# Kernel tuning notes

Measured on AMD Instinct MI355X. Metric: run time of the kernel, lower is better.

The kernel has to match this reference:

```python
import jax, jax.numpy as jnp
import numpy as np

N, D, E, H, O, K = 4096, 1024, 8, 2048, 1024, 2
LOSS_COEF = 0.01


def setup_inputs() -> dict:
    key = jax.random.key(0)
    ks = jax.random.split(key, 8)
    x = jax.random.normal(ks[0], (N, D), jnp.float32)
    return {
        "x": x,
        "x_offsets": jnp.array([0, N // 2, N], jnp.int32),  # unused by forward math
        "max_seq_len": 2048,
        "group_norm": False,
        "num_groups": 8,
        "linear_dim": D // 8,
        "norm_weight": jax.random.uniform(ks[1], (D,), jnp.float32, 0.5, 1.5),
        "norm_bias": jax.random.normal(ks[2], (D,), jnp.float32) * 0.1,
        "norm_eps": 1e-5,
        "w_gate": jax.random.normal(ks[3], (D, E), jnp.float32) * (1.0 / np.sqrt(D)),
        "experts_hidden_w": jax.random.normal(ks[4], (E, H, D), jnp.float32) * 0.02,
        "experts_hidden_bias": jnp.zeros((E, H), jnp.float32),
        "experts_w": jax.random.normal(ks[5], (E, O, H), jnp.float32) * 0.02,
        "experts_bias": jnp.zeros((E, O), jnp.float32),
        "output_weight": jax.random.normal(ks[6], (D, O), jnp.float32) * 0.02,
    }


def _cv_squared(v, eps=1e-6):
    v = v.astype(jnp.float32)
    m = v.mean()
    return jnp.var(v, ddof=1) / (m * m + eps)  # torch .var() is unbiased


def reference(x, x_offsets, max_seq_len, group_norm, num_groups, linear_dim,
              norm_weight, norm_bias, norm_eps,
              w_gate, experts_hidden_w, experts_hidden_bias,
              experts_w, experts_bias, output_weight):
    # ---- input normalization (layer_norm branch; group_norm=False) ----
    if group_norm:
        xg = x.reshape(-1, num_groups, linear_dim)
        mu = xg.mean(axis=2, keepdims=True)
        var = ((xg - mu) ** 2).mean(axis=2, keepdims=True)
        xg = (xg - mu) * jax.lax.rsqrt(var + norm_eps)
        xg = xg * norm_weight[None, :, None] + norm_bias[None, :, None]
        x_norm = xg.reshape(-1, x.shape[-1])
    else:
        mu = x.mean(axis=-1, keepdims=True)
        var = ((x - mu) ** 2).mean(axis=-1, keepdims=True)  # biased, like F.layer_norm
        x_norm = (x - mu) * jax.lax.rsqrt(var + norm_eps) * norm_weight + norm_bias

    # ---- gating: clean logits (enable_noisy_gating=False), L2-normalize rows ----
    logits = x_norm @ w_gate                                  # [N, E]
    logits = logits / jnp.maximum(
        jnp.linalg.norm(logits, axis=1, keepdims=True), 1e-12)
    probs = jax.nn.softmax(logits, axis=1)                    # softmax over all experts
    _, top_idx = jax.lax.top_k(logits, K)                     # [N, K]
    gates_k = jnp.take_along_axis(probs, top_idx, axis=1)     # top-k of softmax(logits)
    rows = jnp.arange(logits.shape[0])[:, None]
    gates = jnp.zeros_like(logits).at[rows, top_idx].set(gates_k)  # [N, E] sparse gates

    # ---- load-balancing loss (train=True, non-noisy path) ----
    importance = gates.sum(axis=0)
    load = (gates > 0).sum(axis=0).astype(jnp.float32)
    loss = (_cv_squared(importance) + _cv_squared(load)) * LOSS_COEF

    # ---- expert MLPs; gates are exactly zero off top-k so masked-dense == dispatch ----
    h = jax.nn.silu(jnp.einsum('nd,ehd->enh', x_norm, experts_hidden_w)
                    + experts_hidden_bias[:, None, :])        # [E, N, H]
    eo = jnp.einsum('enh,eoh->eno', h, experts_w) + experts_bias[:, None, :]  # [E, N, O]
    y_moe = jnp.einsum('ne,eno->no', gates.astype(jnp.float32),
                       eo.astype(jnp.float32))                # fp32 combine, like index_add

    # ---- residual projection: addmm(y_moe, x, output_weight) ----
    y = y_moe + x @ output_weight
    gate_fraction = load / load.sum()
    return (y, loss, gate_fraction)
```

## Files before the change

### kernel.cpp

```cpp
#include <hip/hip_runtime.h>
#include <hip/hip_bf16.h>
#include <stdint.h>

#define N_TOK 4096
#define DIM   1024
#define NE    8
#define NH    2048
#define NO    1024

typedef __attribute__((ext_vector_type(8))) short bf16x8;
typedef __attribute__((ext_vector_type(4))) float f32x4;

__device__ inline unsigned short f2bf(float f) {
    unsigned u = __float_as_uint(f);
    u += 0x7fffu + ((u >> 16) & 1u);
    return (unsigned short)(u >> 16);
}

__device__ inline void async_copy16(const void* g, void* l) {
    __builtin_amdgcn_global_load_lds(
        (const __attribute__((address_space(1))) void*)g,
        (__attribute__((address_space(3))) void*)l, 16, 0, 0);
}

__global__ __launch_bounds__(256) void ln_gate_kernel(
    const float* __restrict__ x, const float* __restrict__ nw,
    const float* __restrict__ nb, const float* __restrict__ eps_p,
    const float* __restrict__ wg,
    unsigned short* __restrict__ xn_bf, unsigned short* __restrict__ x_bf,
    int* __restrict__ tok_e, float* __restrict__ tok_g)
{
    int n = blockIdx.x;
    int t = threadIdx.x;
    int lane = t & 63, wv = t >> 6;

    const float4 xv = ((const float4*)(x + (size_t)n * DIM))[t];
    float s  = xv.x + xv.y + xv.z + xv.w;
    float s2 = xv.x*xv.x + xv.y*xv.y + xv.z*xv.z + xv.w*xv.w;
    #pragma unroll
    for (int o = 32; o > 0; o >>= 1) {
        s  += __shfl_down(s, o);
        s2 += __shfl_down(s2, o);
    }
    __shared__ float rs[4], rs2[4];
    __shared__ float gred[4][NE];
    if (lane == 0) { rs[wv] = s; rs2[wv] = s2; }
    __syncthreads();
    float S  = rs[0] + rs[1] + rs[2] + rs[3];
    float S2 = rs2[0] + rs2[1] + rs2[2] + rs2[3];
    const float inv = 1.0f / (float)DIM;
    float mu = S * inv;
    float var = fmaxf(S2 * inv - mu * mu, 0.0f);
    float rstd = rsqrtf(var + eps_p[0]);

    float4 w4 = ((const float4*)nw)[t];
    float4 b4 = ((const float4*)nb)[t];
    float xn0 = (xv.x - mu) * rstd * w4.x + b4.x;
    float xn1 = (xv.y - mu) * rstd * w4.y + b4.y;
    float xn2 = (xv.z - mu) * rstd * w4.z + b4.z;
    float xn3 = (xv.w - mu) * rstd * w4.w + b4.w;

    ushort4 pn; pn.x = f2bf(xn0); pn.y = f2bf(xn1); pn.z = f2bf(xn2); pn.w = f2bf(xn3);
    ((ushort4*)(xn_bf + (size_t)n * DIM))[t] = pn;
    ushort4 px; px.x = f2bf(xv.x); px.y = f2bf(xv.y); px.z = f2bf(xv.z); px.w = f2bf(xv.w);
    ((ushort4*)(x_bf + (size_t)n * DIM))[t] = px;

    float acc[NE];
    #pragma unroll
    for (int e = 0; e < NE; ++e) acc[e] = 0.0f;
    float xns[4] = {xn0, xn1, xn2, xn3};
    const float4* wgp = (const float4*)(wg + (size_t)(4 * t) * NE);
    #pragma unroll
    for (int j = 0; j < 4; ++j) {
        float4 w0 = wgp[2 * j], w1 = wgp[2 * j + 1];
        float xj = xns[j];
        acc[0] += xj * w0.x; acc[1] += xj * w0.y; acc[2] += xj * w0.z; acc[3] += xj * w0.w;
        acc[4] += xj * w1.x; acc[5] += xj * w1.y; acc[6] += xj * w1.z; acc[7] += xj * w1.w;
    }
    #pragma unroll
    for (int o = 32; o > 0; o >>= 1) {
        #pragma unroll
        for (int e = 0; e < NE; ++e) acc[e] += __shfl_down(acc[e], o);
    }
    if (lane == 0) {
        #pragma unroll
        for (int e = 0; e < NE; ++e) gred[wv][e] = acc[e];
    }
    __syncthreads();
    if (t == 0) {
        float lg[NE];
        float nrm2 = 0.0f;
        #pragma unroll
        for (int e = 0; e < NE; ++e) {
            lg[e] = gred[0][e] + gred[1][e] + gred[2][e] + gred[3][e];
            nrm2 += lg[e] * lg[e];
        }
        float den = fmaxf(sqrtf(nrm2), 1e-12f);
        float linv = 1.0f / den;
        #pragma unroll
        for (int e = 0; e < NE; ++e) lg[e] *= linv;
        float mx = lg[0];
        #pragma unroll
        for (int e = 1; e < NE; ++e) mx = fmaxf(mx, lg[e]);
        float p[NE], ps = 0.0f;
        #pragma unroll
        for (int e = 0; e < NE; ++e) { p[e] = expf(lg[e] - mx); ps += p[e]; }
        float pinv = 1.0f / ps;
        #pragma unroll
        for (int e = 0; e < NE; ++e) p[e] *= pinv;
        int i0 = 0; float b0 = lg[0];
        #pragma unroll
        for (int e = 1; e < NE; ++e) if (lg[e] > b0) { b0 = lg[e]; i0 = e; }
        int i1 = -1; float b1 = -3.0e38f;
        #pragma unroll
        for (int e = 0; e < NE; ++e) if (e != i0 && lg[e] > b1) { b1 = lg[e]; i1 = e; }
        tok_e[2 * n] = i0; tok_e[2 * n + 1] = i1;
        tok_g[2 * n] = p[i0]; tok_g[2 * n + 1] = p[i1];
    }
}

__global__ void cvt_bf16_kernel(const float* __restrict__ src,
                                unsigned short* __restrict__ dst, int n4) {
    int i = blockIdx.x * blockDim.x + threadIdx.x;
    if (i < n4) {
        float4 v = ((const float4*)src)[i];
        ushort4 o; o.x = f2bf(v.x); o.y = f2bf(v.y); o.z = f2bf(v.z); o.w = f2bf(v.w);
        ((ushort4*)dst)[i] = o;
    }
}

__global__ void transpose_cvt_kernel(const float* __restrict__ w,
                                     unsigned short* __restrict__ wt) {
    __shared__ float tile[32][33];
    int tx = threadIdx.x, ty = threadIdx.y;
    int o0 = blockIdx.x * 32, d0 = blockIdx.y * 32;
    tile[ty][tx] = w[(size_t)(d0 + ty) * NO + o0 + tx];
    __syncthreads();
    wt[(size_t)(o0 + ty) * DIM + d0 + tx] = f2bf(tile[tx][ty]);
}

__device__ inline float cv_sq(const float* v) {
    float m = 0.0f;
    for (int e = 0; e < NE; ++e) m += v[e];
    m *= (1.0f / NE);
    float s = 0.0f;
    for (int e = 0; e < NE; ++e) { float d = v[e] - m; s += d * d; }
    s *= (1.0f / (NE - 1));
    return s / (m * m + 1e-6f);
}

__global__ __launch_bounds__(1024) void count_finalize_kernel(
    const int* __restrict__ tok_e, const float* __restrict__ tok_g,
    int* __restrict__ counts, int* __restrict__ offsets,
    int* __restrict__ cursor_pad, float* __restrict__ out_tail)
{
    int t = threadIdx.x;
    int lane = t & 63, wv = t >> 6;
    int lc[NE]; float li[NE];
    #pragma unroll
    for (int e = 0; e < NE; ++e) { lc[e] = 0; li[e] = 0.0f; }
    const int4* ep = (const int4*)(tok_e) + 2 * t;
    const float4* gp = (const float4*)(tok_g) + 2 * t;
    #pragma unroll
    for (int q = 0; q < 2; ++q) {
        int4 e4 = ep[q]; float4 g4 = gp[q];
        lc[e4.x]++; li[e4.x] += g4.x;
        lc[e4.y]++; li[e4.y] += g4.y;
        lc[e4.z]++; li[e4.z] += g4.z;
        lc[e4.w]++; li[e4.w] += g4.w;
    }
    #pragma unroll
    for (int o = 32; o > 0; o >>= 1) {
        #pragma unroll
        for (int e = 0; e < NE; ++e) {
            lc[e] += __shfl_down(lc[e], o);
            li[e] += __shfl_down(li[e], o);
        }
    }
    __shared__ int   sc[16][NE];
    __shared__ float sf[16][NE];
    if (lane == 0) {
        #pragma unroll
        for (int e = 0; e < NE; ++e) { sc[wv][e] = lc[e]; sf[wv][e] = li[e]; }
    }
    __syncthreads();
    if (t == 0) {
        float lif[NE], lcf[NE];
        int off = 0;
        for (int e = 0; e < NE; ++e) {
            int c = 0; float im = 0.0f;
            for (int w = 0; w < 16; ++w) { c += sc[w][e]; im += sf[w][e]; }
            counts[e] = c;
            offsets[e] = off;
            cursor_pad[e * 32] = off;
            off += c;
            lcf[e] = (float)c; lif[e] = im;
        }
        float tot = (float)off;
        out_tail[0] = 0.01f * (cv_sq(lif) + cv_sq(lcf));
        for (int e = 0; e < NE; ++e) out_tail[1 + e] = lcf[e] / tot;
    }
}

__global__ __launch_bounds__(256) void scatter_kernel(
    const int* __restrict__ tok_e, int* __restrict__ cursor_pad,
    int* __restrict__ rowsbuf, int* __restrict__ pair_slot)
{
    __shared__ int lhist[NE];
    __shared__ int lbase[NE];
    int t = threadIdx.x;
    int tok0 = blockIdx.x * 512 + 2 * t;
    if (t < NE) lhist[t] = 0;
    __syncthreads();
    int4 e4 = *(const int4*)(tok_e + 2 * tok0);
    int r0 = atomicAdd(&lhist[e4.x], 1);
    int r1 = atomicAdd(&lhist[e4.y], 1);
    int r2 = atomicAdd(&lhist[e4.z], 1);
    int r3 = atomicAdd(&lhist[e4.w], 1);
    __syncthreads();
    if (t < NE) lbase[t] = atomicAdd(&cursor_pad[t * 32], lhist[t]);
    __syncthreads();
    int s0 = lbase[e4.x] + r0;
    int s1 = lbase[e4.y] + r1;
    int s2 = lbase[e4.z] + r2;
    int s3 = lbase[e4.w] + r3;
    rowsbuf[s0] = tok0;     rowsbuf[s1] = tok0;
    rowsbuf[s2] = tok0 + 1; rowsbuf[s3] = tok0 + 1;
    *(int4*)(pair_slot + 2 * tok0) = (int4){s0, s1, s2, s3};
}

#define BK 64

__global__ __launch_bounds__(256) void gemm1_kernel(
    const unsigned short* __restrict__ xn,
    const unsigned short* __restrict__ wh,
    const float* __restrict__ hb,
    const int* __restrict__ rowsbuf,
    const int* __restrict__ counts, const int* __restrict__ offsets,
    unsigned short* __restrict__ hbuf)
{
    int e = blockIdx.z;
    int count = counts[e];
    int tm = blockIdx.y, tn = blockIdx.x;
    if (tm * 128 >= count) return;
    int off = offsets[e];

    __shared__ alignas(16) short As[128 * BK];
    __shared__ alignas(16) short Bs[128 * BK];

    int t = threadIdx.x;
    int c = t & 7, rl = t >> 3;
    int csw = (c ^ (rl & 7)) * 8;
    const unsigned short* aptr[4];
    const unsigned short* bptr[4];
    #pragma unroll
    for (int p = 0; p < 4; ++p) {
        int mrow = tm * 128 + p * 32 + rl;
        int mc = mrow < count ? mrow : count - 1;
        int token = rowsbuf[off + mc];
        aptr[p] = xn + (size_t)token * DIM;
        bptr[p] = wh + ((size_t)e * NH + tn * 128 + p * 32 + rl) * DIM;
    }

    int lane = t & 63, wvi = t >> 6;
    int wm = (wvi & 1) * 64, wn = (wvi >> 1) * 64;
    int l15 = lane & 15, q = lane >> 4, sw = l15 & 7;

    f32x4 acc[4][4];
    #pragma unroll
    for (int i = 0; i < 4; ++i)
        #pragma unroll
        for (int j = 0; j < 4; ++j) acc[i][j] = (f32x4){0.f, 0.f, 0.f, 0.f};

    for (int kt = 0; kt < DIM / BK; ++kt) {
        int kb = kt * BK + csw;
        #pragma unroll
        for (int p = 0; p < 4; ++p)
            async_copy16(aptr[p] + kb, (char*)As + p * 4096 + t * 16);
        #pragma unroll
        for (int p = 0; p < 4; ++p)
            async_copy16(bptr[p] + kb, (char*)Bs + p * 4096 + t * 16);
        __syncthreads();
        #pragma unroll
        for (int ks = 0; ks < 2; ++ks) {
            int ph = ((ks * 4 + q) ^ sw) * 8;
            bf16x8 af[4], bfr[4];
            #pragma unroll
            for (int i = 0; i < 4; ++i)
                af[i] = *(const bf16x8*)&As[(wm + i * 16 + l15) * BK + ph];
            #pragma unroll
            for (int j = 0; j < 4; ++j)
                bfr[j] = *(const bf16x8*)&Bs[(wn + j * 16 + l15) * BK + ph];
            #pragma unroll
            for (int i = 0; i < 4; ++i)
                #pragma unroll
                for (int j = 0; j < 4; ++j)
                    acc[i][j] = __builtin_amdgcn_mfma_f32_16x16x32_bf16(af[i], bfr[j], acc[i][j], 0, 0, 0);
        }
        __syncthreads();
    }

    int q4 = (lane >> 4) * 4;
    #pragma unroll
    for (int i = 0; i < 4; ++i) {
        #pragma unroll
        for (int r = 0; r < 4; ++r) {
            int m = tm * 128 + wm + i * 16 + q4 + r;
            if (m < count) {
                size_t rowbase = (size_t)(off + m) * NH;
                #pragma unroll
                for (int j = 0; j < 4; ++j) {
                    int col = tn * 128 + wn + j * 16 + l15;
                    float v = acc[i][j][r] + hb[e * NH + col];
                    v = v / (1.0f + __expf(-v));
                    hbuf[rowbase + col] = f2bf(v);
                }
            }
        }
    }
}

__global__ __launch_bounds__(256) void gemm2_kernel(
    const unsigned short* __restrict__ hbuf,
    const unsigned short* __restrict__ wo,
    const float* __restrict__ ob,
    const int* __restrict__ counts, const int* __restrict__ offsets,
    float* __restrict__ eo)
{
    int e = blockIdx.z;
    int count = counts[e];
    int tm = blockIdx.y, tn = blockIdx.x;
    if (tm * 128 >= count) return;
    int off = offsets[e];

    __shared__ alignas(16) short As[128 * BK];
    __shared__ alignas(16) short Bs[64 * BK];

    int t = threadIdx.x;
    int c = t & 7, rl = t >> 3;
    int csw = (c ^ (rl & 7)) * 8;
    const unsigned short* aptr[4];
    const unsigned short* bptr[2];
    #pragma unroll
    for (int p = 0; p < 4; ++p) {
        int mrow = tm * 128 + p * 32 + rl;
        int mc = mrow < count ? mrow : count - 1;
        aptr[p] = hbuf + (size_t)(off + mc) * NH;
    }
    #pragma unroll
    for (int p = 0; p < 2; ++p)
        bptr[p] = wo + ((size_t)e * NO + tn * 64 + p * 32 + rl) * NH;

    int lane = t & 63, wvi = t >> 6;
    int wm = (wvi & 1) * 64, wn = (wvi >> 1) * 32;
    int l15 = lane & 15, q = lane >> 4, sw = l15 & 7;

    f32x4 acc[4][2];
    #pragma unroll
    for (int i = 0; i < 4; ++i)
        #pragma unroll
        for (int j = 0; j < 2; ++j) acc[i][j] = (f32x4){0.f, 0.f, 0.f, 0.f};

    for (int kt = 0; kt < NH / BK; ++kt) {
        int kb = kt * BK + csw;
        #pragma unroll
        for (int p = 0; p < 4; ++p)
            async_copy16(aptr[p] + kb, (char*)As + p * 4096 + t * 16);
        #pragma unroll
        for (int p = 0; p < 2; ++p)
            async_copy16(bptr[p] + kb, (char*)Bs + p * 4096 + t * 16);
        __syncthreads();
        #pragma unroll
        for (int ks = 0; ks < 2; ++ks) {
            int ph = ((ks * 4 + q) ^ sw) * 8;
            bf16x8 af[4], bfr[2];
            #pragma unroll
            for (int i = 0; i < 4; ++i)
                af[i] = *(const bf16x8*)&As[(wm + i * 16 + l15) * BK + ph];
            #pragma unroll
            for (int j = 0; j < 2; ++j)
                bfr[j] = *(const bf16x8*)&Bs[(wn + j * 16 + l15) * BK + ph];
            #pragma unroll
            for (int i = 0; i < 4; ++i)
                #pragma unroll
                for (int j = 0; j < 2; ++j)
                    acc[i][j] = __builtin_amdgcn_mfma_f32_16x16x32_bf16(af[i], bfr[j], acc[i][j], 0, 0, 0);
        }
        __syncthreads();
    }

    int q4 = (lane >> 4) * 4;
    #pragma unroll
    for (int i = 0; i < 4; ++i) {
        #pragma unroll
        for (int r = 0; r < 4; ++r) {
            int m = tm * 128 + wm + i * 16 + q4 + r;
            if (m < count) {
                size_t rowbase = (size_t)(off + m) * NO;
                #pragma unroll
                for (int j = 0; j < 2; ++j) {
                    int col = tn * 64 + wn + j * 16 + l15;
                    eo[rowbase + col] = acc[i][j][r] + ob[e * NO + col];
                }
            }
        }
    }
}

__global__ __launch_bounds__(256) void gemm_res_kernel(
    const unsigned short* __restrict__ xb,
    const unsigned short* __restrict__ wt,
    float* __restrict__ y)
{
    int tm = blockIdx.y, tn = blockIdx.x;
    __shared__ alignas(16) short As[64 * BK];
    __shared__ alignas(16) short Bs[128 * BK];

    int t = threadIdx.x;
    int c = t & 7, rl = t >> 3;
    int csw = (c ^ (rl & 7)) * 8;
    const unsigned short* aptr[2];
    const unsigned short* bptr[4];
    #pragma unroll
    for (int p = 0; p < 2; ++p)
        aptr[p] = xb + (size_t)(tm * 64 + p * 32 + rl) * DIM;
    #pragma unroll
    for (int p = 0; p < 4; ++p)
        bptr[p] = wt + (size_t)(tn * 128 + p * 32 + rl) * DIM;

    int lane = t & 63, wvi = t >> 6;
    int wm = (wvi & 1) * 32, wn = (wvi >> 1) * 64;
    int l15 = lane & 15, q = lane >> 4, sw = l15 & 7;

    f32x4 acc[2][4];
    #pragma unroll
    for (int i = 0; i < 2; ++i)
        #pragma unroll
        for (int j = 0; j < 4; ++j) acc[i][j] = (f32x4){0.f, 0.f, 0.f, 0.f};

    for (int kt = 0; kt < DIM / BK; ++kt) {
        int kb = kt * BK + csw;
        #pragma unroll
        for (int p = 0; p < 2; ++p)
            async_copy16(aptr[p] + kb, (char*)As + p * 4096 + t * 16);
        #pragma unroll
        for (int p = 0; p < 4; ++p)
            async_copy16(bptr[p] + kb, (char*)Bs + p * 4096 + t * 16);
        __syncthreads();
        #pragma unroll
        for (int ks = 0; ks < 2; ++ks) {
            int ph = ((ks * 4 + q) ^ sw) * 8;
            bf16x8 af[2], bfr[4];
            #pragma unroll
            for (int i = 0; i < 2; ++i)
                af[i] = *(const bf16x8*)&As[(wm + i * 16 + l15) * BK + ph];
            #pragma unroll
            for (int j = 0; j < 4; ++j)
                bfr[j] = *(const bf16x8*)&Bs[(wn + j * 16 + l15) * BK + ph];
            #pragma unroll
            for (int i = 0; i < 2; ++i)
                #pragma unroll
                for (int j = 0; j < 4; ++j)
                    acc[i][j] = __builtin_amdgcn_mfma_f32_16x16x32_bf16(af[i], bfr[j], acc[i][j], 0, 0, 0);
        }
        __syncthreads();
    }

    int q4 = (lane >> 4) * 4;
    #pragma unroll
    for (int i = 0; i < 2; ++i) {
        #pragma unroll
        for (int r = 0; r < 4; ++r) {
            int row = tm * 64 + wm + i * 16 + q4 + r;
            #pragma unroll
            for (int j = 0; j < 4; ++j) {
                int col = tn * 128 + wn + j * 16 + l15;
                y[(size_t)row * NO + col] = acc[i][j][r];
            }
        }
    }
}

__global__ __launch_bounds__(256) void combine_kernel(
    float* __restrict__ y, const float* __restrict__ eo,
    const int* __restrict__ pair_slot, const float* __restrict__ tok_g)
{
    int n = blockIdx.x, t = threadIdx.x;
    int s0 = pair_slot[2 * n], s1 = pair_slot[2 * n + 1];
    float g0 = tok_g[2 * n], g1 = tok_g[2 * n + 1];
    float4 a = ((const float4*)(eo + (size_t)s0 * NO))[t];
    float4 b = ((const float4*)(eo + (size_t)s1 * NO))[t];
    float4* yp = (float4*)(y + (size_t)n * NO) + t;
    float4 v = *yp;
    v.x += g0 * a.x + g1 * b.x;
    v.y += g0 * a.y + g1 * b.y;
    v.z += g0 * a.z + g1 * b.z;
    v.w += g0 * a.w + g1 * b.w;
    *yp = v;
}

extern "C" void kernel_launch(void* const* d_in, const int* in_sizes, int n_in,
                              void* d_out, int out_size, void* d_ws, size_t ws_size,
                              hipStream_t stream) {
    const float* x    = (const float*)d_in[0];
    const float* nw   = (const float*)d_in[6];
    const float* nb   = (const float*)d_in[7];
    const float* eps  = (const float*)d_in[8];
    const float* wg   = (const float*)d_in[9];
    const float* whw  = (const float*)d_in[10];
    const float* whb  = (const float*)d_in[11];
    const float* wow  = (const float*)d_in[12];
    const float* wob  = (const float*)d_in[13];
    const float* wout = (const float*)d_in[14];

    char* ws = (char*)d_ws;
    unsigned short* xn_bf = (unsigned short*)(ws + 0);
    unsigned short* x_bf  = (unsigned short*)(ws + 8388608);
    unsigned short* wh_bf = (unsigned short*)(ws + 16777216);
    float*          eo    = (float*)(ws + 16777216);
    unsigned short* wo_bf = (unsigned short*)(ws + 50331648);
    unsigned short* wt_bf = (unsigned short*)(ws + 83886080);
    unsigned short* hbuf  = (unsigned short*)(ws + 85983232);
    char* meta = ws + 119537664;
    int*   counts     = (int*)(meta + 0);
    int*   offsets    = (int*)(meta + 128);
    int*   cursor_pad = (int*)(meta + 256);
    int*   tok_e      = (int*)(meta + 2048);
    float* tok_g      = (float*)(meta + 2048 + 32768);
    int*   rowsbuf    = (int*)(meta + 2048 + 65536);
    int*   pair_slot  = (int*)(meta + 2048 + 98304);

    float* y = (float*)d_out;
    float* out_tail = y + (size_t)N_TOK * NO;

    ln_gate_kernel<<<N_TOK, 256, 0, stream>>>(x, nw, nb, eps, wg, xn_bf, x_bf,
                                              tok_e, tok_g);
    {
        int n4 = NE * NH * DIM / 4;
        cvt_bf16_kernel<<<n4 / 256, 256, 0, stream>>>(whw, wh_bf, n4);
        cvt_bf16_kernel<<<n4 / 256, 256, 0, stream>>>(wow, wo_bf, n4);
    }
    transpose_cvt_kernel<<<dim3(NO / 32, DIM / 32), dim3(32, 32), 0, stream>>>(wout, wt_bf);
    count_finalize_kernel<<<1, 1024, 0, stream>>>(tok_e, tok_g, counts, offsets,
                                                  cursor_pad, out_tail);
    scatter_kernel<<<N_TOK / 512, 256, 0, stream>>>(tok_e, cursor_pad, rowsbuf, pair_slot);
    gemm1_kernel<<<dim3(NH / 128, N_TOK / 128, NE), 256, 0, stream>>>(
        xn_bf, wh_bf, whb, rowsbuf, counts, offsets, hbuf);
    gemm2_kernel<<<dim3(NO / 64, N_TOK / 128, NE), 256, 0, stream>>>(
        hbuf, wo_bf, wob, counts, offsets, eo);
    gemm_res_kernel<<<dim3(NO / 128, N_TOK / 64), 256, 0, stream>>>(x_bf, wt_bf, y);
    combine_kernel<<<N_TOK, 256, 0, stream>>>(y, eo, pair_slot, tok_g);
}
```

Before: 403.0 us.

## Use 32x32x16 MFMA in GEMMs, fuse routing kernels and weight conversions

All three GEMM kernels move from 16x16x32 bf16 MFMA tiles to 32x32x16 tiles with 16-wide accumulators, which cuts the number of LDS fragment loads and MFMA issues per K step. The count/finalize and scatter kernels merge into one multi-block route kernel. Each block recomputes the global histogram and writes deterministic slots through LDS atomics, avoiding global atomics and a launch. The two weight-conversion launches are merged into one. The epilogue store pattern changes to the 32x32 accumulator layout, which may give less coalesced writes.

```diff
diff --git a/kernel.cpp b/kernel.cpp
--- a/kernel.cpp
+++ b/kernel.cpp
@@ -9,7 +9,7 @@
 #define NO    1024
 
 typedef __attribute__((ext_vector_type(8))) short bf16x8;
-typedef __attribute__((ext_vector_type(4))) float f32x4;
+typedef __attribute__((ext_vector_type(16))) float f32x16;
 
 __device__ inline unsigned short f2bf(float f) {
     unsigned u = __float_as_uint(f);
@@ -119,14 +119,16 @@
     }
 }
 
-__global__ void cvt_bf16_kernel(const float* __restrict__ src,
-                                unsigned short* __restrict__ dst, int n4) {
+__global__ void cvt2_bf16_kernel(const float* __restrict__ a, unsigned short* __restrict__ da,
+                                 const float* __restrict__ b, unsigned short* __restrict__ db,
+                                 int n4each) {
     int i = blockIdx.x * blockDim.x + threadIdx.x;
-    if (i < n4) {
-        float4 v = ((const float4*)src)[i];
-        ushort4 o; o.x = f2bf(v.x); o.y = f2bf(v.y); o.z = f2bf(v.z); o.w = f2bf(v.w);
-        ((ushort4*)dst)[i] = o;
-    }
+    const float4* s; ushort4* d; int j;
+    if (i < n4each) { s = (const float4*)a; d = (ushort4*)da; j = i; }
+    else            { s = (const float4*)b; d = (ushort4*)db; j = i - n4each; }
+    float4 v = s[j];
+    ushort4 o; o.x = f2bf(v.x); o.y = f2bf(v.y); o.z = f2bf(v.z); o.w = f2bf(v.w);
+    d[j] = o;
 }
 
 __global__ void transpose_cvt_kernel(const float* __restrict__ w,
@@ -149,84 +151,84 @@
     return s / (m * m + 1e-6f);
 }
 
-__global__ __launch_bounds__(1024) void count_finalize_kernel(
+__global__ __launch_bounds__(256) void route_kernel(
     const int* __restrict__ tok_e, const float* __restrict__ tok_g,
     int* __restrict__ counts, int* __restrict__ offsets,
-    int* __restrict__ cursor_pad, float* __restrict__ out_tail)
+    int* __restrict__ rowsbuf, int* __restrict__ pair_slot,
+    float* __restrict__ out_tail)
 {
-    int t = threadIdx.x;
+    int b = blockIdx.x, t = threadIdx.x;
     int lane = t & 63, wv = t >> 6;
+    int chunk0 = b * 1024;
+
     int lc[NE]; float li[NE];
     #pragma unroll
     for (int e = 0; e < NE; ++e) { lc[e] = 0; li[e] = 0.0f; }
-    const int4* ep = (const int4*)(tok_e) + 2 * t;
-    const float4* gp = (const float4*)(tok_g) + 2 * t;
-    #pragma unroll
-    for (int q = 0; q < 2; ++q) {
-        int4 e4 = ep[q]; float4 g4 = gp[q];
+    int base = t * 32;
+    #pragma unroll
+    for (int q = 0; q < 8; ++q) {
+        int4 e4 = *(const int4*)(tok_e + base + q * 4);
+        float4 g4 = *(const float4*)(tok_g + base + q * 4);
         lc[e4.x]++; li[e4.x] += g4.x;
         lc[e4.y]++; li[e4.y] += g4.y;
         lc[e4.z]++; li[e4.z] += g4.z;
         lc[e4.w]++; li[e4.w] += g4.w;
     }
+    int prior_flag = (base + 32 <= chunk0) ? 1 : 0;
+    int lp[NE];
+    #pragma unroll
+    for (int e = 0; e < NE; ++e) lp[e] = prior_flag ? lc[e] : 0;
+
     #pragma unroll
     for (int o = 32; o > 0; o >>= 1) {
         #pragma unroll
         for (int e = 0; e < NE; ++e) {
             lc[e] += __shfl_down(lc[e], o);
+            lp[e] += __shfl_down(lp[e], o);
             li[e] += __shfl_down(li[e], o);
         }
     }
-    __shared__ int   sc[16][NE];
-    __shared__ float sf[16][NE];
+    __shared__ int   sc[4][NE], sp[4][NE];
+    __shared__ float sf[4][NE];
+    __shared__ int   lcur[NE];
     if (lane == 0) {
         #pragma unroll
-        for (int e = 0; e < NE; ++e) { sc[wv][e] = lc[e]; sf[wv][e] = li[e]; }
+        for (int e = 0; e < NE; ++e) { sc[wv][e] = lc[e]; sp[wv][e] = lp[e]; sf[wv][e] = li[e]; }
     }
     __syncthreads();
     if (t == 0) {
-        float lif[NE], lcf[NE];
+        int cnt[NE], pri[NE]; float imp[NE];
+        for (int e = 0; e < NE; ++e) {
+            cnt[e] = sc[0][e] + sc[1][e] + sc[2][e] + sc[3][e];
+            pri[e] = sp[0][e] + sp[1][e] + sp[2][e] + sp[3][e];
+            imp[e] = sf[0][e] + sf[1][e] + sf[2][e] + sf[3][e];
+        }
         int off = 0;
         for (int e = 0; e < NE; ++e) {
-            int c = 0; float im = 0.0f;
-            for (int w = 0; w < 16; ++w) { c += sc[w][e]; im += sf[w][e]; }
-            counts[e] = c;
-            offsets[e] = off;
-            cursor_pad[e * 32] = off;
-            off += c;
-            lcf[e] = (float)c; lif[e] = im;
-        }
-        float tot = (float)off;
-        out_tail[0] = 0.01f * (cv_sq(lif) + cv_sq(lcf));
-        for (int e = 0; e < NE; ++e) out_tail[1 + e] = lcf[e] / tot;
-    }
-}
-
-__global__ __launch_bounds__(256) void scatter_kernel(
-    const int* __restrict__ tok_e, int* __restrict__ cursor_pad,
-    int* __restrict__ rowsbuf, int* __restrict__ pair_slot)
-{
-    __shared__ int lhist[NE];
-    __shared__ int lbase[NE];
-    int t = threadIdx.x;
-    int tok0 = blockIdx.x * 512 + 2 * t;
-    if (t < NE) lhist[t] = 0;
+            lcur[e] = off + pri[e];
+            if (b == 0) { counts[e] = cnt[e]; offsets[e] = off; }
+            off += cnt[e];
+        }
+        if (b == 0) {
+            float lcf[NE], lif[NE];
+            for (int e = 0; e < NE; ++e) { lcf[e] = (float)cnt[e]; lif[e] = imp[e]; }
+            float tot = (float)off;
+            out_tail[0] = 0.01f * (cv_sq(lif) + cv_sq(lcf));
+            for (int e = 0; e < NE; ++e) out_tail[1 + e] = lcf[e] / tot;
+        }
+    }
     __syncthreads();
-    int4 e4 = *(const int4*)(tok_e + 2 * tok0);
-    int r0 = atomicAdd(&lhist[e4.x], 1);
-    int r1 = atomicAdd(&lhist[e4.y], 1);
-    int r2 = atomicAdd(&lhist[e4.z], 1);
-    int r3 = atomicAdd(&lhist[e4.w], 1);
-    __syncthreads();
-    if (t < NE) lbase[t] = atomicAdd(&cursor_pad[t * 32], lhist[t]);
-    __syncthreads();
-    int s0 = lbase[e4.x] + r0;
-    int s1 = lbase[e4.y] + r1;
-    int s2 = lbase[e4.z] + r2;
-    int s3 = lbase[e4.w] + r3;
+
+    int g0 = chunk0 + 4 * t;
+    int4 e4 = *(const int4*)(tok_e + g0);
+    int s0 = atomicAdd(&lcur[e4.x], 1);
+    int s1 = atomicAdd(&lcur[e4.y], 1);
+    int s2 = atomicAdd(&lcur[e4.z], 1);
+    int s3 = atomicAdd(&lcur[e4.w], 1);
+    int tok0 = g0 >> 1;
     rowsbuf[s0] = tok0;     rowsbuf[s1] = tok0;
     rowsbuf[s2] = tok0 + 1; rowsbuf[s3] = tok0 + 1;
-    *(int4*)(pair_slot + 2 * tok0) = (int4){s0, s1, s2, s3};
+    *(int4*)(pair_slot + g0) = (int4){s0, s1, s2, s3};
 }
 
 #define BK 64
@@ -264,13 +266,13 @@
 
     int lane = t & 63, wvi = t >> 6;
     int wm = (wvi & 1) * 64, wn = (wvi >> 1) * 64;
-    int l15 = lane & 15, q = lane >> 4, sw = l15 & 7;
-
-    f32x4 acc[4][4];
-    #pragma unroll
-    for (int i = 0; i < 4; ++i)
-        #pragma unroll
-        for (int j = 0; j < 4; ++j) acc[i][j] = (f32x4){0.f, 0.f, 0.f, 0.f};
+    int l31 = lane & 31, h = lane >> 5, sw = l31 & 7;
+
+    f32x16 acc[2][2];
+    #pragma unroll
+    for (int i = 0; i < 2; ++i)
+        #pragma unroll
+        for (int j = 0; j < 2; ++j) acc[i][j] = (f32x16)(0.0f);
 
     for (int kt = 0; kt < DIM / BK; ++kt) {
         int kb = kt * BK + csw;
@@ -282,38 +284,38 @@
             async_copy16(bptr[p] + kb, (char*)Bs + p * 4096 + t * 16);
         __syncthreads();
         #pragma unroll
-        for (int ks = 0; ks < 2; ++ks) {
-            int ph = ((ks * 4 + q) ^ sw) * 8;
-            bf16x8 af[4], bfr[4];
-            #pragma unroll
-            for (int i = 0; i < 4; ++i)
-                af[i] = *(const bf16x8*)&As[(wm + i * 16 + l15) * BK + ph];
-            #pragma unroll
-            for (int j = 0; j < 4; ++j)
-                bfr[j] = *(const bf16x8*)&Bs[(wn + j * 16 + l15) * BK + ph];
-            #pragma unroll
-            for (int i = 0; i < 4; ++i)
+        for (int ks = 0; ks < 4; ++ks) {
+            int ph = ((ks * 2 + h) ^ sw) * 8;
+            bf16x8 af[2], bfr[2];
+            #pragma unroll
+            for (int i = 0; i < 2; ++i)
+                af[i] = *(const bf16x8*)&As[(wm + i * 32 + l31) * BK + ph];
+            #pragma unroll
+            for (int j = 0; j < 2; ++j)
+                bfr[j] = *(const bf16x8*)&Bs[(wn + j * 32 + l31) * BK + ph];
+            #pragma unroll
+            for (int i = 0; i < 2; ++i)
                 #pragma unroll
-                for (int j = 0; j < 4; ++j)
-                    acc[i][j] = __builtin_amdgcn_mfma_f32_16x16x32_bf16(af[i], bfr[j], acc[i][j], 0, 0, 0);
+                for (int j = 0; j < 2; ++j)
+                    acc[i][j] = __builtin_amdgcn_mfma_f32_32x32x16_bf16(af[i], bfr[j], acc[i][j], 0, 0, 0);
         }
         __syncthreads();
     }
 
-    int q4 = (lane >> 4) * 4;
-    #pragma unroll
-    for (int i = 0; i < 4; ++i) {
-        #pragma unroll
-        for (int r = 0; r < 4; ++r) {
-            int m = tm * 128 + wm + i * 16 + q4 + r;
-            if (m < count) {
-                size_t rowbase = (size_t)(off + m) * NH;
-                #pragma unroll
-                for (int j = 0; j < 4; ++j) {
-                    int col = tn * 128 + wn + j * 16 + l15;
-                    float v = acc[i][j][r] + hb[e * NH + col];
+    #pragma unroll
+    for (int i = 0; i < 2; ++i) {
+        #pragma unroll
+        for (int j = 0; j < 2; ++j) {
+            int col = tn * 128 + wn + j * 32 + l31;
+            float bias = hb[e * NH + col];
+            #pragma unroll
+            for (int r = 0; r < 16; ++r) {
+                int row_d = (r & 3) + 8 * (r >> 2) + 4 * h;
+                int m = tm * 128 + wm + i * 32 + row_d;
+                if (m < count) {
+                    float v = acc[i][j][r] + bias;
                     v = v / (1.0f + __expf(-v));
-                    hbuf[rowbase + col] = f2bf(v);
+                    hbuf[(size_t)(off + m) * NH + col] = f2bf(v);
                 }
             }
         }
@@ -353,13 +355,11 @@
 
     int lane = t & 63, wvi = t >> 6;
     int wm = (wvi & 1) * 64, wn = (wvi >> 1) * 32;
-    int l15 = lane & 15, q = lane >> 4, sw = l15 & 7;
-
-    f32x4 acc[4][2];
-    #pragma unroll
-    for (int i = 0; i < 4; ++i)
-        #pragma unroll
-        for (int j = 0; j < 2; ++j) acc[i][j] = (f32x4){0.f, 0.f, 0.f, 0.f};
+    int l31 = lane & 31, h = lane >> 5, sw = l31 & 7;
+
+    f32x16 acc[2];
+    #pragma unroll
+    for (int i = 0; i < 2; ++i) acc[i] = (f32x16)(0.0f);
 
     for (int kt = 0; kt < NH / BK; ++kt) {
         int kb = kt * BK + csw;
@@ -371,38 +371,30 @@
             async_copy16(bptr[p] + kb, (char*)Bs + p * 4096 + t * 16);
         __syncthreads();
         #pragma unroll
-        for (int ks = 0; ks < 2; ++ks) {
-            int ph = ((ks * 4 + q) ^ sw) * 8;
-            bf16x8 af[4], bfr[2];
-            #pragma unroll
-            for (int i = 0; i < 4; ++i)
-                af[i] = *(const bf16x8*)&As[(wm + i * 16 + l15) * BK + ph];
-            #pragma unroll
-            for (int j = 0; j < 2; ++j)
-                bfr[j] = *(const bf16x8*)&Bs[(wn + j * 16 + l15) * BK + ph];
-            #pragma unroll
-            for (int i = 0; i < 4; ++i)
-                #pragma unroll
-                for (int j = 0; j < 2; ++j)
-                    acc[i][j] = __builtin_amdgcn_mfma_f32_16x16x32_bf16(af[i], bfr[j], acc[i][j], 0, 0, 0);
+        for (int ks = 0; ks < 4; ++ks) {
+            int ph = ((ks * 2 + h) ^ sw) * 8;
+            bf16x8 af[2], bfr;
+            #pragma unroll
+            for (int i = 0; i < 2; ++i)
+                af[i] = *(const bf16x8*)&As[(wm + i * 32 + l31) * BK + ph];
+            bfr = *(const bf16x8*)&Bs[(wn + l31) * BK + ph];
+            #pragma unroll
+            for (int i = 0; i < 2; ++i)
+                acc[i] = __builtin_amdgcn_mfma_f32_32x32x16_bf16(af[i], bfr, acc[i], 0, 0, 0);
         }
         __syncthreads();
     }
 
-    int q4 = (lane >> 4) * 4;
-    #pragma unroll
-    for (int i = 0; i < 4; ++i) {
-        #pragma unroll
-        for (int r = 0; r < 4; ++r) {
-            int m = tm * 128 + wm + i * 16 + q4 + r;
-            if (m < count) {
-                size_t rowbase = (size_t)(off + m) * NO;
-                #pragma unroll
-                for (int j = 0; j < 2; ++j) {
-                    int col = tn * 64 + wn + j * 16 + l15;
-                    eo[rowbase + col] = acc[i][j][r] + ob[e * NO + col];
-                }
-            }
+    int col = tn * 64 + wn + l31;
+    float bias = ob[e * NO + col];
+    #pragma unroll
+    for (int i = 0; i < 2; ++i) {
+        #pragma unroll
+        for (int r = 0; r < 16; ++r) {
+            int row_d = (r & 3) + 8 * (r >> 2) + 4 * h;
+            int m = tm * 128 + wm + i * 32 + row_d;
+            if (m < count)
+                eo[(size_t)(off + m) * NO + col] = acc[i][r] + bias;
         }
     }
 }
@@ -430,13 +422,11 @@
 
     int lane = t & 63, wvi = t >> 6;
     int wm = (wvi & 1) * 32, wn = (wvi >> 1) * 64;
-    int l15 = lane & 15, q = lane >> 4, sw = l15 & 7;
-
-    f32x4 acc[2][4];
-    #pragma unroll
-    for (int i = 0; i < 2; ++i)
-        #pragma unroll
-        for (int j = 0; j < 4; ++j) acc[i][j] = (f32x4){0.f, 0.f, 0.f, 0.f};
+    int l31 = lane & 31, h = lane >> 5, sw = l31 & 7;
+
+    f32x16 acc[2];
+    #pragma unroll
+    for (int j = 0; j < 2; ++j) acc[j] = (f32x16)(0.0f);
 
     for (int kt = 0; kt < DIM / BK; ++kt) {
         int kb = kt * BK + csw;
@@ -448,35 +438,28 @@
             async_copy16(bptr[p] + kb, (char*)Bs + p * 4096 + t * 16);
         __syncthreads();
         #pragma unroll
-        for (int ks = 0; ks < 2; ++ks) {
-            int ph = ((ks * 4 + q) ^ sw) * 8;
-            bf16x8 af[2], bfr[4];
-            #pragma unroll
-            for (int i = 0; i < 2; ++i)
-                af[i] = *(const bf16x8*)&As[(wm + i * 16 + l15) * BK + ph];
-            #pragma unroll
-            for (int j = 0; j < 4; ++j)
-                bfr[j] = *(const bf16x8*)&Bs[(wn + j * 16 + l15) * BK + ph];
-            #pragma unroll
-            for (int i = 0; i < 2; ++i)
-                #pragma unroll
-                for (int j = 0; j < 4; ++j)
-                    acc[i][j] = __builtin_amdgcn_mfma_f32_16x16x32_bf16(af[i], bfr[j], acc[i][j], 0, 0, 0);
+        for (int ks = 0; ks < 4; ++ks) {
+            int ph = ((ks * 2 + h) ^ sw) * 8;
+            bf16x8 af, bfr[2];
+            af = *(const bf16x8*)&As[(wm + l31) * BK + ph];
+            #pragma unroll
+            for (int j = 0; j < 2; ++j)
+                bfr[j] = *(const bf16x8*)&Bs[(wn + j * 32 + l31) * BK + ph];
+            #pragma unroll
+            for (int j = 0; j < 2; ++j)
+                acc[j] = __builtin_amdgcn_mfma_f32_32x32x16_bf16(af, bfr[j], acc[j], 0, 0, 0);
         }
         __syncthreads();
     }
 
-    int q4 = (lane >> 4) * 4;
-    #pragma unroll
-    for (int i = 0; i < 2; ++i) {
-        #pragma unroll
-        for (int r = 0; r < 4; ++r) {
-            int row = tm * 64 + wm + i * 16 + q4 + r;
-            #pragma unroll
-            for (int j = 0; j < 4; ++j) {
-                int col = tn * 128 + wn + j * 16 + l15;
-                y[(size_t)row * NO + col] = acc[i][j][r];
-            }
+    #pragma unroll
+    for (int j = 0; j < 2; ++j) {
+        int col = tn * 128 + wn + j * 32 + l31;
+        #pragma unroll
+        for (int r = 0; r < 16; ++r) {
+            int row_d = (r & 3) + 8 * (r >> 2) + 4 * h;
+            int row = tm * 64 + wm + row_d;
+            y[(size_t)row * NO + col] = acc[j][r];
         }
     }
 }
@@ -524,7 +507,6 @@
     char* meta = ws + 119537664;
     int*   counts     = (int*)(meta + 0);
     int*   offsets    = (int*)(meta + 128);
-    int*   cursor_pad = (int*)(meta + 256);
     int*   tok_e      = (int*)(meta + 2048);
     float* tok_g      = (float*)(meta + 2048 + 32768);
     int*   rowsbuf    = (int*)(meta + 2048 + 65536);
@@ -537,13 +519,11 @@
                                               tok_e, tok_g);
     {
         int n4 = NE * NH * DIM / 4;
-        cvt_bf16_kernel<<<n4 / 256, 256, 0, stream>>>(whw, wh_bf, n4);
-        cvt_bf16_kernel<<<n4 / 256, 256, 0, stream>>>(wow, wo_bf, n4);
+        cvt2_bf16_kernel<<<2 * n4 / 256, 256, 0, stream>>>(whw, wh_bf, wow, wo_bf, n4);
     }
     transpose_cvt_kernel<<<dim3(NO / 32, DIM / 32), dim3(32, 32), 0, stream>>>(wout, wt_bf);
-    count_finalize_kernel<<<1, 1024, 0, stream>>>(tok_e, tok_g, counts, offsets,
-                                                  cursor_pad, out_tail);
-    scatter_kernel<<<N_TOK / 512, 256, 0, stream>>>(tok_e, cursor_pad, rowsbuf, pair_slot);
+    route_kernel<<<NE, 256, 0, stream>>>(tok_e, tok_g, counts, offsets,
+                                         rowsbuf, pair_slot, out_tail);
     gemm1_kernel<<<dim3(NH / 128, N_TOK / 128, NE), 256, 0, stream>>>(
         xn_bf, wh_bf, whb, rowsbuf, counts, offsets, hbuf);
     gemm2_kernel<<<dim3(NO / 64, N_TOK / 128, NE), 256, 0, stream>>>(
```

Result: faster. 389.1 us (-3.5%).
